# Optimization experiments

Hardware: AMD Instinct MI355X
Metric: run time of the kernel (lower is better)

## Reference

```python
import jax, jax.numpy as jnp
import numpy as np

B, K, C, O = 8, 100000, 16, 16
HG, WG = 512, 512
ALPHA_PRIOR = 1.0
KERN = np.array([[0.075, 0.125, 0.075], [0.125, 0.3, 0.125], [0.075, 0.125, 0.075]], dtype=np.float32)


def setup_inputs() -> dict:
    key = jax.random.key(0)
    k1, k2, k3, k4, k5 = jax.random.split(key, 5)
    node_feat = jax.random.normal(k1, (B, K, C), dtype=jnp.float32)
    node_xy = jax.random.uniform(k2, (B, K, 2), dtype=jnp.float32, minval=0.0, maxval=WG - 1.0)
    node_types = jax.random.randint(k3, (B, K), 0, 2)
    # kaiming_normal_ fan_out: std = sqrt(2 / fan_out), fan_out = O*1*1
    std = (2.0 / O) ** 0.5
    w_obj = jax.random.normal(k4, (O, C), dtype=jnp.float32) * std
    w_prior = jax.random.normal(k5, (O, C), dtype=jnp.float32) * std
    hw = np.array([HG, WG], dtype=np.int64)
    return {"node_feat": node_feat, "node_xy": node_xy, "hw": hw,
            "node_types": node_types, "w_obj": w_obj, "w_prior": w_prior}


def rasterize(node_feat, node_xy, weight, H, W):
    # node_feat [B,K,C], node_xy [B,K,2], weight [B,K] 0/1 mask (masked scatter == scatter of zeros)
    xs = jnp.clip(jnp.round(node_xy[..., 0]), 0, W - 1).astype(jnp.int32)
    ys = jnp.clip(jnp.round(node_xy[..., 1]), 0, H - 1).astype(jnp.int32)
    idx = ys * W + xs  # [B,K] flat grid index
    src = node_feat * weight[..., None]  # zero out non-selected nodes

    def scat(idx_b, src_b):
        return jnp.zeros((H * W, src_b.shape[-1]), src_b.dtype).at[idx_b].add(src_b)

    grid = jax.vmap(scat)(idx, src)  # [B,HW,C]
    return grid.reshape(grid.shape[0], H, W, -1).transpose(0, 3, 1, 2)  # [B,C,H,W]


def splat3x3(x, kern):
    # depthwise 3x3 conv, groups = C
    c = x.shape[1]
    w = jnp.broadcast_to(kern[None, None], (c, 1, 3, 3))
    return jax.lax.conv_general_dilated(
        x, w, window_strides=(1, 1), padding='SAME',
        dimension_numbers=('NCHW', 'OIHW', 'NCHW'), feature_group_count=c)


def reference(node_feat, node_xy, hw, node_types, w_obj, w_prior):
    H, W = int(hw[0]), int(hw[1])
    kern = jnp.asarray(KERN)
    mask_obj = (node_types == 0).astype(node_feat.dtype)
    mask_prior = (node_types == 1).astype(node_feat.dtype)
    map_obj = splat3x3(rasterize(node_feat, node_xy, mask_obj, H, W), kern)
    map_prior = splat3x3(rasterize(node_feat, node_xy, mask_prior, H, W), kern)
    # rasterize + splat run under torch.no_grad() in the original
    map_obj = jax.lax.stop_gradient(map_obj)
    map_prior = jax.lax.stop_gradient(map_prior)
    out = jnp.einsum('oc,bchw->bohw', w_obj, map_obj) \
        + ALPHA_PRIOR * jnp.einsum('oc,bchw->bohw', w_prior, map_prior)
    return out
```

## Files before the change

kernel.cpp:

```cpp
#include <hip/hip_runtime.h>

#define B_ 8
#define K_ 100000
#define NODES (B_ * K_)
#define C_ 16
#define O_ 16
#define H_ 512
#define W_ 512
#define TSX 32
#define TSY 16
#define NTX (W_ / TSX)
#define NTY (H_ / TSY)
#define NBKT (B_ * NTX * NTY)
#define CAP 512
#define EX (TSX + 2)
#define EY (TSY + 2)
#define PLANE (EX * EY)

#define FB 1000
#define FPB (FB / B_)
#define FCHUNK (K_ / FPB)

#define CURP 16
#define CUR_BYTES (NBKT * CURP * 4)
#define IDS_OFF CUR_BYTES
#define P_OFF (IDS_OFF + NBKT * CAP * 4)
#define WS_NEED_PRE ((size_t)P_OFF + (size_t)NODES * O_ * 4)

__device__ __forceinline__ float bf_lo(unsigned int u) {
    union { unsigned int i; float f; } v; v.i = u << 16; return v.f;
}
__device__ __forceinline__ float bf_hi(unsigned int u) {
    union { unsigned int i; float f; } v; v.i = u & 0xffff0000u; return v.f;
}
__device__ __forceinline__ unsigned short f2bf(float f) {
    union { float f; unsigned int u; } v; v.f = f;
    unsigned int u = v.u;
    u += 0x7fffu + ((u >> 16) & 1u);
    return (unsigned short)(u >> 16);
}

__device__ __forceinline__ int probe_fp32_ballot(const unsigned int* xy) {
    const int lane = threadIdx.x & 63;
    int bad = 0;
    #pragma unroll
    for (int k = 0; k < 4; ++k) {
        float lo = bf_lo(xy[lane + (k << 6)]);
        bad |= !(lo >= 0.0f && lo <= 512.0f);
    }
    return __ballot(bad) != 0ull;
}

__device__ __forceinline__ void decode_xy(const void* xy, int fp32, int n,
                                          int& xs, int& ys)
{
    float x, y;
    if (fp32) { float2 p = ((const float2*)xy)[n]; x = p.x; y = p.y; }
    else { unsigned int u = ((const unsigned int*)xy)[n]; x = bf_lo(u); y = bf_hi(u); }
    xs = min(max((int)rintf(x), 0), W_ - 1);
    ys = min(max((int)rintf(y), 0), H_ - 1);
}

__device__ __forceinline__ void load_feat16(const void* feat, size_t n, int fp32,
                                            float* f)
{
    if (fp32) {
        const float4* ff = (const float4*)feat + n * 4;
        float4 a = ff[0], b2 = ff[1], c = ff[2], d = ff[3];
        f[0]=a.x; f[1]=a.y; f[2]=a.z; f[3]=a.w;
        f[4]=b2.x; f[5]=b2.y; f[6]=b2.z; f[7]=b2.w;
        f[8]=c.x; f[9]=c.y; f[10]=c.z; f[11]=c.w;
        f[12]=d.x; f[13]=d.y; f[14]=d.z; f[15]=d.w;
    } else {
        const uint4* ff = (const uint4*)feat + n * 2;
        uint4 A = ff[0], Bv = ff[1];
        f[0]=bf_lo(A.x);  f[1]=bf_hi(A.x);  f[2]=bf_lo(A.y);  f[3]=bf_hi(A.y);
        f[4]=bf_lo(A.z);  f[5]=bf_hi(A.z);  f[6]=bf_lo(A.w);  f[7]=bf_hi(A.w);
        f[8]=bf_lo(Bv.x); f[9]=bf_hi(Bv.x); f[10]=bf_lo(Bv.y); f[11]=bf_hi(Bv.y);
        f[12]=bf_lo(Bv.z); f[13]=bf_hi(Bv.z); f[14]=bf_lo(Bv.w); f[15]=bf_hi(Bv.w);
    }
}

__device__ __forceinline__ void load_weights_lds(float* wl, int fp32,
                                                 const void* w_obj,
                                                 const void* w_prior,
                                                 int tid, int nthreads)
{
    for (int i = tid; i < 2 * O_ * C_; i += nthreads) {
        if (fp32) {
            wl[i] = (i < O_ * C_) ? ((const float*)w_obj)[i]
                                  : ((const float*)w_prior)[i - O_ * C_];
        } else {
            unsigned short raw = (i < O_ * C_)
                ? ((const unsigned short*)w_obj)[i]
                : ((const unsigned short*)w_prior)[i - O_ * C_];
            union { unsigned int u; float f; } v; v.u = ((unsigned int)raw) << 16;
            wl[i] = v.f;
        }
    }
}

template<bool PRE>
__global__ __launch_bounds__(256) void fill_bins(
    const void* __restrict__ feat, const void* __restrict__ xy,
    const int* __restrict__ types,
    const void* __restrict__ w_obj, const void* __restrict__ w_prior,
    int* __restrict__ cursor, int* __restrict__ ids, float* __restrict__ p)
{
    __shared__ int hist[NTX * NTY];
    __shared__ unsigned int rec[FCHUNK];
    __shared__ float wl[PRE ? 2 * O_ * C_ : 2];

    const int tid = threadIdx.x;
    const int fp32 = probe_fp32_ballot((const unsigned int*)xy);
    for (int j = tid; j < NTX * NTY; j += 256) hist[j] = 0;
    if constexpr (PRE) load_weights_lds(wl, fp32, w_obj, w_prior, tid, 256);
    __syncthreads();

    const int bb = blockIdx.x / FPB;
    const int local0 = (blockIdx.x % FPB) * FCHUNK;
    const int s = bb * K_ + local0;

    for (int ii = tid; ii < FCHUNK; ii += 256) {
        const int n = s + ii;
        int xs, ys; decode_xy(xy, fp32, n, xs, ys);
        const int t = (types[n] != 0);
        rec[ii] = (unsigned)(xs | (ys << 9) | (t << 18));

        if constexpr (PRE) {
            float f[16];
            load_feat16(feat, (size_t)n, fp32, f);
            const float* wrow = &wl[t * O_ * C_];
            float pv[16];
            #pragma unroll
            for (int o = 0; o < O_; ++o) {
                float acc = 0.f;
                #pragma unroll
                for (int c = 0; c < C_; ++c) acc = fmaf(wrow[o * C_ + c], f[c], acc);
                pv[o] = acc;
            }
            float4* pout = (float4*)(p + (size_t)n * O_);
            pout[0] = make_float4(pv[0],  pv[1],  pv[2],  pv[3]);
            pout[1] = make_float4(pv[4],  pv[5],  pv[6],  pv[7]);
            pout[2] = make_float4(pv[8],  pv[9],  pv[10], pv[11]);
            pout[3] = make_float4(pv[12], pv[13], pv[14], pv[15]);
        }

        int xlo = max((xs - 1) >> 5, 0), xhi = min((xs + 1) >> 5, NTX - 1);
        int ylo = max((ys - 1) >> 4, 0), yhi = min((ys + 1) >> 4, NTY - 1);
        for (int tyy = ylo; tyy <= yhi; ++tyy)
            for (int txx = xlo; txx <= xhi; ++txx)
                atomicAdd(&hist[tyy * NTX + txx], 1);
    }
    __syncthreads();

    for (int j = tid; j < NTX * NTY; j += 256) {
        int c = hist[j];
        hist[j] = c ? atomicAdd(&cursor[(bb * NTX * NTY + j) * CURP], c) : 0;
    }
    __syncthreads();

    for (int ii = tid; ii < FCHUNK; ii += 256) {
        unsigned r = rec[ii];
        int xs = r & 511, ys = (r >> 9) & 511, t = (r >> 18) & 1;
        int local = local0 + ii;
        int xlo = max((xs - 1) >> 5, 0), xhi = min((xs + 1) >> 5, NTX - 1);
        int ylo = max((ys - 1) >> 4, 0), yhi = min((ys + 1) >> 4, NTY - 1);
        for (int tyy = ylo; tyy <= yhi; ++tyy)
            for (int txx = xlo; txx <= xhi; ++txx) {
                int bk = tyy * NTX + txx;
                int slot = atomicAdd(&hist[bk], 1);
                if (slot < CAP) {
                    int lx = xs - (txx << 5) + 1;
                    int ly = ys - (tyy << 4) + 1;
                    ids[(bb * NTX * NTY + bk) * CAP + slot] =
                        local | (t << 17) | (lx << 18) | (ly << 24);
                }
            }
    }
}

template<bool PRE>
__global__ __launch_bounds__(512) void tile_fused(
    const void* __restrict__ src ,
    const void* __restrict__ xy,
    const void* __restrict__ w_obj, const void* __restrict__ w_prior,
    const int* __restrict__ cursor, const int* __restrict__ ids,
    void* __restrict__ out)
{
    __shared__ float accs[O_ * PLANE];
    __shared__ float wl[PRE ? 2 : 2 * O_ * C_];

    const int tid = threadIdx.x;
    const int tx = blockIdx.x, ty = blockIdx.y, b = blockIdx.z;
    const int bucket = (b * NTY + ty) * NTX + tx;
    int cnt = cursor[bucket * CURP];
    if (cnt > CAP) cnt = CAP;
    const int fp32 = probe_fp32_ballot((const unsigned int*)xy);

    const int node = ((tid & 7) << 6) | (tid >> 3);
    const unsigned pck = (unsigned)ids[bucket * CAP + node];
    const int local = pck & 0x1FFFF;
    const int t  = (pck >> 17) & 1;
    const int lx = (pck >> 18) & 63;
    const int ly = (pck >> 24) & 31;
    const bool active = (node < cnt);

    float f[16];
    if (active) {
        const size_t n = (size_t)b * K_ + local;
        if constexpr (PRE) {
            const float4* pp = (const float4*)src + n * 4;
            float4 a = pp[0], b2 = pp[1], c = pp[2], d = pp[3];
            f[0]=a.x; f[1]=a.y; f[2]=a.z; f[3]=a.w;
            f[4]=b2.x; f[5]=b2.y; f[6]=b2.z; f[7]=b2.w;
            f[8]=c.x; f[9]=c.y; f[10]=c.z; f[11]=c.w;
            f[12]=d.x; f[13]=d.y; f[14]=d.z; f[15]=d.w;
        } else {
            load_feat16(src, n, fp32, f);
        }
    }

    for (int i = tid; i < O_ * PLANE; i += 512) accs[i] = 0.f;
    if constexpr (!PRE) load_weights_lds(wl, fp32, w_obj, w_prior, tid, 512);
    __syncthreads();

    if (active) {
        float* cell = &accs[ly * EX + lx];
        if constexpr (PRE) {
            #pragma unroll
            for (int o = 0; o < O_; ++o) atomicAdd(cell + o * PLANE, f[o]);
        } else {
            const float* wrow = &wl[t * O_ * C_];
            #pragma unroll
            for (int o = 0; o < O_; ++o) {
                float acc = 0.f;
                #pragma unroll
                for (int c = 0; c < C_; ++c) acc = fmaf(wrow[o * C_ + c], f[c], acc);
                atomicAdd(cell + o * PLANE, acc);
            }
        }
    }
    __syncthreads();

    const int x = tid & 31;
    const int o = tid >> 5;
    const float* pl = &accs[o * PLANE + x];
    float hA2 = 0.f, hA1 = 0.f, hB1 = 0.f;
    const int x0 = tx * TSX, y0 = ty * TSY;
    const size_t obase = (((size_t)(b * O_ + o)) * H_) * W_;

    #pragma unroll
    for (int iy = 0; iy < EY; ++iy) {
        float l = pl[iy * EX], c = pl[iy * EX + 1], r = pl[iy * EX + 2];
        float sfx = l + r;
        float hA = fmaf(0.075f, sfx, 0.125f * c);
        float hB = fmaf(0.125f, sfx, 0.3f * c);
        if (iy >= 2) {
            float v = hA2 + hB1 + hA;
            size_t oi = obase + (size_t)(y0 + iy - 2) * W_ + (x0 + x);
            if (fp32) ((float*)out)[oi] = v;
            else      ((unsigned short*)out)[oi] = f2bf(v);
        }
        hA2 = hA1; hA1 = hA; hB1 = hB;
    }
}

extern "C" void kernel_launch(void* const* d_in, const int* in_sizes, int n_in,
                              void* d_out, int out_size, void* d_ws, size_t ws_size,
                              hipStream_t stream)
{
    const void* feat = d_in[0];
    const void* xy = d_in[1];
    const int* types = (const int*)d_in[3];
    const void* w_obj = d_in[4];
    const void* w_prior = d_in[5];

    int* cursor = (int*)d_ws;
    int* ids = (int*)((char*)d_ws + IDS_OFF);
    float* p = (float*)((char*)d_ws + P_OFF);

    hipMemsetAsync(cursor, 0, CUR_BYTES, stream);
    if (ws_size >= WS_NEED_PRE) {
        fill_bins<true><<<FB, 256, 0, stream>>>(feat, xy, types, w_obj, w_prior,
                                                cursor, ids, p);
        tile_fused<true><<<dim3(NTX, NTY, B_), 512, 0, stream>>>(
            p, xy, w_obj, w_prior, cursor, ids, d_out);
    } else {
        fill_bins<false><<<FB, 256, 0, stream>>>(feat, xy, types, w_obj, w_prior,
                                                 cursor, ids, p);
        tile_fused<false><<<dim3(NTX, NTY, B_), 512, 0, stream>>>(
            feat, xy, w_obj, w_prior, cursor, ids, d_out);
    }
}
```

Before: 306.2 us.

## Split projection and binning into separate block roles with direct global atomics

Replaces the chunked fill_bins kernel, which built an LDS histogram and reserved bucket ranges in two passes, with one kernel whose blocks take one of two roles. Some blocks only project node features through the weights, and the others bin nodes by atomically incrementing global bucket cursors directly, once per touched tile. This removes the two-pass LDS histogram, its barriers and the recompute, and lets projection and binning run concurrently. In exchange it adds many more global atomics, and the order of ids within a bucket is no longer deterministic. Output stores are also made nontemporal.

```diff
diff --git a/kernel.cpp b/kernel.cpp
--- a/kernel.cpp
+++ b/kernel.cpp
@@ -17,9 +17,9 @@
 #define EY (TSY + 2)
 #define PLANE (EX * EY)
 
-#define FB 1000
-#define FPB (FB / B_)
-#define FCHUNK (K_ / FPB)
+#define PROJ_BLKS 1536
+#define BIN_BLKS 512
+#define TOTAL_BLKS (PROJ_BLKS + BIN_BLKS)
 
 #define CURP 16
 #define CUR_BYTES (NBKT * CURP * 4)
@@ -101,33 +101,24 @@
 }
 
 template<bool PRE>
-__global__ __launch_bounds__(256) void fill_bins(
+__global__ __launch_bounds__(256, 8) void proj_bin(
     const void* __restrict__ feat, const void* __restrict__ xy,
     const int* __restrict__ types,
     const void* __restrict__ w_obj, const void* __restrict__ w_prior,
     int* __restrict__ cursor, int* __restrict__ ids, float* __restrict__ p)
 {
-    __shared__ int hist[NTX * NTY];
-    __shared__ unsigned int rec[FCHUNK];
-    __shared__ float wl[PRE ? 2 * O_ * C_ : 2];
-
     const int tid = threadIdx.x;
+    const int blk = blockIdx.x;
     const int fp32 = probe_fp32_ballot((const unsigned int*)xy);
-    for (int j = tid; j < NTX * NTY; j += 256) hist[j] = 0;
-    if constexpr (PRE) load_weights_lds(wl, fp32, w_obj, w_prior, tid, 256);
-    __syncthreads();
-
-    const int bb = blockIdx.x / FPB;
-    const int local0 = (blockIdx.x % FPB) * FCHUNK;
-    const int s = bb * K_ + local0;
-
-    for (int ii = tid; ii < FCHUNK; ii += 256) {
-        const int n = s + ii;
-        int xs, ys; decode_xy(xy, fp32, n, xs, ys);
-        const int t = (types[n] != 0);
-        rec[ii] = (unsigned)(xs | (ys << 9) | (t << 18));
-
-        if constexpr (PRE) {
+
+    if (blk < PROJ_BLKS) {
+        if constexpr (!PRE) return;
+        __shared__ float wl[2 * O_ * C_];
+        load_weights_lds(wl, fp32, w_obj, w_prior, tid, 256);
+        __syncthreads();
+
+        for (int n = blk * 256 + tid; n < NODES; n += PROJ_BLKS * 256) {
+            const int t = (types[n] != 0);
             float f[16];
             load_feat16(feat, (size_t)n, fp32, f);
             const float* wrow = &wl[t * O_ * C_];
@@ -145,38 +136,27 @@
             pout[2] = make_float4(pv[8],  pv[9],  pv[10], pv[11]);
             pout[3] = make_float4(pv[12], pv[13], pv[14], pv[15]);
         }
-
-        int xlo = max((xs - 1) >> 5, 0), xhi = min((xs + 1) >> 5, NTX - 1);
-        int ylo = max((ys - 1) >> 4, 0), yhi = min((ys + 1) >> 4, NTY - 1);
-        for (int tyy = ylo; tyy <= yhi; ++tyy)
-            for (int txx = xlo; txx <= xhi; ++txx)
-                atomicAdd(&hist[tyy * NTX + txx], 1);
-    }
-    __syncthreads();
-
-    for (int j = tid; j < NTX * NTY; j += 256) {
-        int c = hist[j];
-        hist[j] = c ? atomicAdd(&cursor[(bb * NTX * NTY + j) * CURP], c) : 0;
-    }
-    __syncthreads();
-
-    for (int ii = tid; ii < FCHUNK; ii += 256) {
-        unsigned r = rec[ii];
-        int xs = r & 511, ys = (r >> 9) & 511, t = (r >> 18) & 1;
-        int local = local0 + ii;
-        int xlo = max((xs - 1) >> 5, 0), xhi = min((xs + 1) >> 5, NTX - 1);
-        int ylo = max((ys - 1) >> 4, 0), yhi = min((ys + 1) >> 4, NTY - 1);
-        for (int tyy = ylo; tyy <= yhi; ++tyy)
-            for (int txx = xlo; txx <= xhi; ++txx) {
-                int bk = tyy * NTX + txx;
-                int slot = atomicAdd(&hist[bk], 1);
-                if (slot < CAP) {
-                    int lx = xs - (txx << 5) + 1;
-                    int ly = ys - (tyy << 4) + 1;
-                    ids[(bb * NTX * NTY + bk) * CAP + slot] =
-                        local | (t << 17) | (lx << 18) | (ly << 24);
+    } else {
+        const int j0 = (blk - PROJ_BLKS) * 256 + tid;
+        for (int n = j0; n < NODES; n += BIN_BLKS * 256) {
+            const int b = n / K_;
+            const int local = n - b * K_;
+            int xs, ys; decode_xy(xy, fp32, n, xs, ys);
+            const int t = (types[n] != 0);
+            const int xlo = max((xs - 1) >> 5, 0), xhi = min((xs + 1) >> 5, NTX - 1);
+            const int ylo = max((ys - 1) >> 4, 0), yhi = min((ys + 1) >> 4, NTY - 1);
+            for (int tyy = ylo; tyy <= yhi; ++tyy)
+                for (int txx = xlo; txx <= xhi; ++txx) {
+                    const int bkg = (b * NTY + tyy) * NTX + txx;
+                    const int slot = atomicAdd(&cursor[bkg * CURP], 1);
+                    if (slot < CAP) {
+                        const int lx = xs - (txx << 5) + 1;
+                        const int ly = ys - (tyy << 4) + 1;
+                        ids[bkg * CAP + slot] =
+                            local | (t << 17) | (lx << 18) | (ly << 24);
+                    }
                 }
-            }
+        }
     }
 }
 
@@ -259,8 +239,8 @@
         if (iy >= 2) {
             float v = hA2 + hB1 + hA;
             size_t oi = obase + (size_t)(y0 + iy - 2) * W_ + (x0 + x);
-            if (fp32) ((float*)out)[oi] = v;
-            else      ((unsigned short*)out)[oi] = f2bf(v);
+            if (fp32) __builtin_nontemporal_store(v, (float*)out + oi);
+            else      __builtin_nontemporal_store(f2bf(v), (unsigned short*)out + oi);
         }
         hA2 = hA1; hA1 = hA; hB1 = hB;
     }
@@ -282,13 +262,13 @@
 
     hipMemsetAsync(cursor, 0, CUR_BYTES, stream);
     if (ws_size >= WS_NEED_PRE) {
-        fill_bins<true><<<FB, 256, 0, stream>>>(feat, xy, types, w_obj, w_prior,
-                                                cursor, ids, p);
+        proj_bin<true><<<TOTAL_BLKS, 256, 0, stream>>>(
+            feat, xy, types, w_obj, w_prior, cursor, ids, p);
         tile_fused<true><<<dim3(NTX, NTY, B_), 512, 0, stream>>>(
             p, xy, w_obj, w_prior, cursor, ids, d_out);
     } else {
-        fill_bins<false><<<FB, 256, 0, stream>>>(feat, xy, types, w_obj, w_prior,
-                                                 cursor, ids, p);
+        proj_bin<false><<<TOTAL_BLKS, 256, 0, stream>>>(
+            feat, xy, types, w_obj, w_prior, cursor, ids, p);
         tile_fused<false><<<dim3(NTX, NTY, B_), 512, 0, stream>>>(
             feat, xy, w_obj, w_prior, cursor, ids, d_out);
     }
```

After: 352.2 us. +15.0%, slower.
